# Optimization experiments

Hardware: AMD Instinct MI355X
Metric: run time of the kernel (lower is better)

Reference implementation:

```python
import jax, jax.numpy as jnp
import numpy as np

B, D = 200000, 128
K = 1024


def setup_inputs() -> dict:
    key = jax.random.key(0)
    k1, k2 = jax.random.split(key)
    x_BD = jax.random.normal(k1, (B, D), dtype=jnp.float32)
    codebook = jax.random.uniform(k2, (K, D), dtype=jnp.float32)
    return {"x_BD": x_BD, "codebook": codebook}


def reference(x_BD, codebook):
    x_sq_B1 = jnp.sum(x_BD * x_BD, axis=-1, keepdims=True)
    c_sq_K = jnp.sum(codebook * codebook, axis=-1)
    dists_BK = x_sq_B1 - 2.0 * jnp.einsum("bd,kd->bk", x_BD, codebook) + c_sq_K
    codes_B = jnp.argmin(dists_BK, axis=-1)  # [B] int
    quant_x_BD = codebook[codes_B]           # gather, [B, D]
    return quant_x_BD, codes_B
```

## Files before the change

kernel.cpp:

```cpp
#include <hip/hip_runtime.h>


typedef float v2f __attribute__((ext_vector_type(2)));

#define DDIM 128
#define KCODES 1024
#define BM 64
#define BN 128
#define DCH 32
#define NTILES (KCODES / BN)
#define NCHUNK (DDIM / DCH)

__global__ void csq_kernel(const float* __restrict__ cb, float* __restrict__ csq) {
    int k = blockIdx.x * blockDim.x + threadIdx.x;
    if (k >= KCODES) return;
    const float* __restrict__ c = cb + (long)k * DDIM;
    float s0 = 0.f, s1 = 0.f, s2 = 0.f, s3 = 0.f;
#pragma unroll
    for (int d = 0; d < DDIM; d += 4) {
        s0 = fmaf(c[d + 0], c[d + 0], s0);
        s1 = fmaf(c[d + 1], c[d + 1], s1);
        s2 = fmaf(c[d + 2], c[d + 2], s2);
        s3 = fmaf(c[d + 3], c[d + 3], s3);
    }
    csq[k] = (s0 + s1) + (s2 + s3);
}

__launch_bounds__(256, 3)
__global__ void vq_gemm_kernel(const float* __restrict__ x, const float* __restrict__ cb,
                               const float* __restrict__ csq, float* __restrict__ quant,
                               float* __restrict__ codes) {
    __shared__ float xs[DDIM * BM];
    __shared__ float cs[DCH * BN];
    __shared__ int win[BM];

    const int tid = threadIdx.x;
    const long r0 = (long)blockIdx.x * BM;

    {
        const int r = tid >> 2;
        const int qb = (tid & 3) * 8;
        const float* __restrict__ xrow = x + (r0 + r) * DDIM;
#pragma unroll
        for (int j = 0; j < 8; ++j) {
            const int q = qb + j;
            const float4 v = *(const float4*)(xrow + q * 4);
            xs[(q * 4 + 0) * BM + r] = v.x;
            xs[(q * 4 + 1) * BM + r] = v.y;
            xs[(q * 4 + 2) * BM + r] = v.z;
            xs[(q * 4 + 3) * BM + r] = v.w;
        }
    }
    __syncthreads();

    const int tr = tid >> 4;
    const int tc = tid & 15;

    float s[4][4];
#pragma unroll
    for (int a = 0; a < 4; ++a)
#pragma unroll
        for (int b = 0; b < 4; ++b) s[a][b] = 0.f;
#pragma unroll
    for (int d = 0; d < DDIM; d += 4) {
#pragma unroll
        for (int dd = 0; dd < 4; ++dd) {
            const float4 v = *(const float4*)&xs[(d + dd) * BM + tr * 4];
            s[dd][0] = fmaf(v.x, v.x, s[dd][0]);
            s[dd][1] = fmaf(v.y, v.y, s[dd][1]);
            s[dd][2] = fmaf(v.z, v.z, s[dd][2]);
            s[dd][3] = fmaf(v.w, v.w, s[dd][3]);
        }
    }
    float xsq[4];
#pragma unroll
    for (int i = 0; i < 4; ++i) xsq[i] = (s[0][i] + s[1][i]) + (s[2][i] + s[3][i]);

    float best[4];
    int bidx[4];
#pragma unroll
    for (int i = 0; i < 4; ++i) { best[i] = 3.4e38f; bidx[i] = 0; }

    for (int ct = 0; ct < NTILES; ++ct) {
        v2f acc[4][4];
#pragma unroll
        for (int i = 0; i < 4; ++i)
#pragma unroll
            for (int jj = 0; jj < 4; ++jj) acc[i][jj] = (v2f){0.f, 0.f};

        for (int dc = 0; dc < NCHUNK; ++dc) {
            __syncthreads();
            {
                const int k = tid >> 1;
                const int qb = (tid & 1) * 4;
                const float* __restrict__ crow =
                    cb + (long)(ct * BN + k) * DDIM + dc * DCH;
#pragma unroll
                for (int j = 0; j < 4; ++j) {
                    const int q = qb + j;
                    const float4 v = *(const float4*)(crow + q * 4);
                    cs[(q * 4 + 0) * BN + k] = v.x;
                    cs[(q * 4 + 1) * BN + k] = v.y;
                    cs[(q * 4 + 2) * BN + k] = v.z;
                    cs[(q * 4 + 3) * BN + k] = v.w;
                }
            }
            __syncthreads();
#pragma unroll
            for (int d = 0; d < DCH; ++d) {
                const float4 xa  = *(const float4*)&xs[(dc * DCH + d) * BM + tr * 4];
                const float4 ca  = *(const float4*)&cs[d * BN + tc * 4];
                const float4 cb2 = *(const float4*)&cs[d * BN + 64 + tc * 4];
                const float xv[4] = {xa.x, xa.y, xa.z, xa.w};
                v2f cv[4];
                cv[0] = (v2f){ca.x, ca.y};
                cv[1] = (v2f){ca.z, ca.w};
                cv[2] = (v2f){cb2.x, cb2.y};
                cv[3] = (v2f){cb2.z, cb2.w};
#pragma unroll
                for (int i = 0; i < 4; ++i) {
                    const v2f xb = (v2f){xv[i], xv[i]};
#pragma unroll
                    for (int jj = 0; jj < 4; ++jj)
                        acc[i][jj] = __builtin_elementwise_fma(xb, cv[jj], acc[i][jj]);
                }
            }
        }

        float csq_r[8];
#pragma unroll
        for (int j = 0; j < 4; ++j) {
            csq_r[j]     = csq[ct * BN + tc * 4 + j];
            csq_r[4 + j] = csq[ct * BN + 64 + tc * 4 + j];
        }
#pragma unroll
        for (int i = 0; i < 4; ++i) {
#pragma unroll
            for (int jj = 0; jj < 4; ++jj) {
#pragma unroll
                for (int h = 0; h < 2; ++h) {
                    const int jl = jj * 2 + h;
                    const int cj = ct * BN + ((jl < 4) ? (tc * 4 + jl) : (64 + tc * 4 + jl - 4));
                    const float dist = fmaf(-2.0f, acc[i][jj][h], xsq[i]) + csq_r[jl];
                    if (dist < best[i]) { best[i] = dist; bidx[i] = cj; }
                }
            }
        }
    }

    __syncthreads();
    float* redb = cs;
    int* redi = (int*)cs + BM * 16;
#pragma unroll
    for (int i = 0; i < 4; ++i) {
        const int r = tr * 4 + i;
        redb[r * 16 + tc] = best[i];
        redi[r * 16 + tc] = bidx[i];
    }
    __syncthreads();
    if (tid < BM) {
        float b = redb[tid * 16];
        int bi = redi[tid * 16];
#pragma unroll
        for (int e = 1; e < 16; ++e) {
            const float v = redb[tid * 16 + e];
            const int vi = redi[tid * 16 + e];
            if (v < b || (v == b && vi < bi)) { b = v; bi = vi; }
        }
        codes[r0 + tid] = (float)bi;
        win[tid] = bi;
    }
    __syncthreads();

    {
        const int r = tid >> 2;
        const int qb = (tid & 3) * 8;
        const float* __restrict__ crow = cb + (long)win[r] * DDIM;
        float* __restrict__ qrow = quant + (r0 + r) * DDIM;
#pragma unroll
        for (int j = 0; j < 8; ++j) {
            const int q = qb + j;
            *(float4*)(qrow + q * 4) = *(const float4*)(crow + q * 4);
        }
    }
}

extern "C" void kernel_launch(void* const* d_in, const int* in_sizes, int n_in,
                              void* d_out, int out_size, void* d_ws, size_t ws_size,
                              hipStream_t stream) {
    const float* x  = (const float*)d_in[0];
    const float* cb = (const float*)d_in[1];
    const int B = in_sizes[0] / DDIM;

    float* quant = (float*)d_out;
    float* codes = (float*)d_out + (size_t)B * DDIM;
    float* csq   = (float*)d_ws;

    csq_kernel<<<(KCODES + 255) / 256, 256, 0, stream>>>(cb, csq);

    const int blocks = B / BM;
    vq_gemm_kernel<<<blocks, 256, 0, stream>>>(x, cb, csq, quant, codes);
}
```

Before: 815.5 us.

## Rewrite VQ kernel with scalar-loaded x rows and transposed codebook streaming

```diff
diff --git a/kernel.cpp b/kernel.cpp
--- a/kernel.cpp
+++ b/kernel.cpp
@@ -2,14 +2,11 @@
 
 
 typedef float v2f __attribute__((ext_vector_type(2)));
+typedef int   v2i __attribute__((ext_vector_type(2)));
 
 #define DDIM 128
 #define KCODES 1024
-#define BM 64
-#define BN 128
-#define DCH 32
-#define NTILES (KCODES / BN)
-#define NCHUNK (DDIM / DCH)
+#define BMR 16
 
 __global__ void csq_kernel(const float* __restrict__ cb, float* __restrict__ csq) {
     int k = blockIdx.x * blockDim.x + threadIdx.x;
@@ -26,162 +23,167 @@
     csq[k] = (s0 + s1) + (s2 + s3);
 }
 
-__launch_bounds__(256, 3)
-__global__ void vq_gemm_kernel(const float* __restrict__ x, const float* __restrict__ cb,
-                               const float* __restrict__ csq, float* __restrict__ quant,
-                               float* __restrict__ codes) {
-    __shared__ float xs[DDIM * BM];
-    __shared__ float cs[DCH * BN];
-    __shared__ int win[BM];
+__global__ void ct_kernel(const float* __restrict__ cb, float* __restrict__ cT) {
+    const int idx = blockIdx.x * 256 + threadIdx.x;
+    const int d = idx >> 10, k = idx & 1023;
+    cT[idx] = cb[k * DDIM + d];
+}
+
+#define PKL(a, xx, cc) \
+    asm("v_pk_fma_f32 %0, %1, %2, %0 op_sel:[0,0,0] op_sel_hi:[0,1,1]" \
+        : "+v"(a) : "s"(xx), "v"(cc))
+#define PKH(a, xx, cc) \
+    asm("v_pk_fma_f32 %0, %1, %2, %0 op_sel:[1,0,0] op_sel_hi:[1,1,1]" \
+        : "+v"(a) : "s"(xx), "v"(cc))
+
+#define DECLX(S) v2i xq##S##0, xq##S##1, xq##S##2, xq##S##3, \
+                     xq##S##4, xq##S##5, xq##S##6, xq##S##7;
+
+#define ISSUE_X(S, xbp) do { const float* _xb = (xbp); \
+    asm volatile( \
+        "s_load_dwordx2 %[a0], %[xb], 0x0\n\t" \
+        "s_load_dwordx2 %[a1], %[xb], 0x200\n\t" \
+        "s_load_dwordx2 %[a2], %[xb], 0x400\n\t" \
+        "s_load_dwordx2 %[a3], %[xb], 0x600\n\t" \
+        "s_load_dwordx2 %[a4], %[xb], 0x800\n\t" \
+        "s_load_dwordx2 %[a5], %[xb], 0xa00\n\t" \
+        "s_load_dwordx2 %[a6], %[xb], 0xc00\n\t" \
+        "s_load_dwordx2 %[a7], %[xb], 0xe00" \
+        : [a0] "=s"(xq##S##0), [a1] "=s"(xq##S##1), \
+          [a2] "=s"(xq##S##2), [a3] "=s"(xq##S##3), \
+          [a4] "=s"(xq##S##4), [a5] "=s"(xq##S##5), \
+          [a6] "=s"(xq##S##6), [a7] "=s"(xq##S##7) \
+        : [xb] "s"(_xb)); } while (0)
+
+#define CROW_L(S, R) \
+    PKL(acc[R][0], xq##S##R, c##S##0); PKL(acc[R][1], xq##S##R, c##S##1); \
+    PKL(acc[R][2], xq##S##R, c##S##2); PKL(acc[R][3], xq##S##R, c##S##3);
+#define CROW_H(S, R) \
+    PKH(acc[R][0], xq##S##R, c##S##4); PKH(acc[R][1], xq##S##R, c##S##5); \
+    PKH(acc[R][2], xq##S##R, c##S##6); PKH(acc[R][3], xq##S##R, c##S##7);
+
+#define COMPUTE(S) do { \
+    CROW_L(S, 0) CROW_L(S, 1) CROW_L(S, 2) CROW_L(S, 3) \
+    CROW_L(S, 4) CROW_L(S, 5) CROW_L(S, 6) CROW_L(S, 7) \
+    CROW_H(S, 0) CROW_H(S, 1) CROW_H(S, 2) CROW_H(S, 3) \
+    CROW_H(S, 4) CROW_H(S, 5) CROW_H(S, 6) CROW_H(S, 7) } while (0)
+
+__launch_bounds__(256, 4)
+__global__ void vq_kernel(const float* __restrict__ x, const float* __restrict__ cb,
+                          const float* __restrict__ cT, const float* __restrict__ csq,
+                          float* __restrict__ quant, float* __restrict__ codes) {
+    __shared__ float xsqs[BMR];
+    __shared__ float redv[4][8];
+    __shared__ int   redi[4][8];
+    __shared__ int   win[BMR];
 
     const int tid = threadIdx.x;
-    const long r0 = (long)blockIdx.x * BM;
-
-    {
-        const int r = tid >> 2;
-        const int qb = (tid & 3) * 8;
-        const float* __restrict__ xrow = x + (r0 + r) * DDIM;
-#pragma unroll
-        for (int j = 0; j < 8; ++j) {
-            const int q = qb + j;
-            const float4 v = *(const float4*)(xrow + q * 4);
-            xs[(q * 4 + 0) * BM + r] = v.x;
-            xs[(q * 4 + 1) * BM + r] = v.y;
-            xs[(q * 4 + 2) * BM + r] = v.z;
-            xs[(q * 4 + 3) * BM + r] = v.w;
+    const int lane = tid & 63;
+    const int wv = __builtin_amdgcn_readfirstlane(tid >> 6);
+    const int rg = wv >> 1;
+    const int ch = wv & 1;
+    const long r0 = (long)blockIdx.x * BMR;
+
+    if (tid < BMR) {
+        const float* __restrict__ xr = x + (r0 + tid) * DDIM;
+        float s0 = 0.f, s1 = 0.f, s2 = 0.f, s3 = 0.f;
+#pragma unroll
+        for (int q = 0; q < 32; ++q) {
+            const float4 v = *(const float4*)(xr + q * 4);
+            s0 = fmaf(v.x, v.x, s0);
+            s1 = fmaf(v.y, v.y, s1);
+            s2 = fmaf(v.z, v.z, s2);
+            s3 = fmaf(v.w, v.w, s3);
         }
+        xsqs[tid] = (s0 + s1) + (s2 + s3);
     }
     __syncthreads();
 
-    const int tr = tid >> 4;
-    const int tc = tid & 15;
-
-    float s[4][4];
-#pragma unroll
-    for (int a = 0; a < 4; ++a)
-#pragma unroll
-        for (int b = 0; b < 4; ++b) s[a][b] = 0.f;
-#pragma unroll
-    for (int d = 0; d < DDIM; d += 4) {
-#pragma unroll
-        for (int dd = 0; dd < 4; ++dd) {
-            const float4 v = *(const float4*)&xs[(d + dd) * BM + tr * 4];
-            s[dd][0] = fmaf(v.x, v.x, s[dd][0]);
-            s[dd][1] = fmaf(v.y, v.y, s[dd][1]);
-            s[dd][2] = fmaf(v.z, v.z, s[dd][2]);
-            s[dd][3] = fmaf(v.w, v.w, s[dd][3]);
-        }
-    }
-    float xsq[4];
-#pragma unroll
-    for (int i = 0; i < 4; ++i) xsq[i] = (s[0][i] + s[1][i]) + (s[2][i] + s[3][i]);
-
-    float best[4];
-    int bidx[4];
-#pragma unroll
-    for (int i = 0; i < 4; ++i) { best[i] = 3.4e38f; bidx[i] = 0; }
-
-    for (int ct = 0; ct < NTILES; ++ct) {
-        v2f acc[4][4];
-#pragma unroll
-        for (int i = 0; i < 4; ++i)
-#pragma unroll
-            for (int jj = 0; jj < 4; ++jj) acc[i][jj] = (v2f){0.f, 0.f};
-
-        for (int dc = 0; dc < NCHUNK; ++dc) {
-            __syncthreads();
-            {
-                const int k = tid >> 1;
-                const int qb = (tid & 1) * 4;
-                const float* __restrict__ crow =
-                    cb + (long)(ct * BN + k) * DDIM + dc * DCH;
-#pragma unroll
-                for (int j = 0; j < 4; ++j) {
-                    const int q = qb + j;
-                    const float4 v = *(const float4*)(crow + q * 4);
-                    cs[(q * 4 + 0) * BN + k] = v.x;
-                    cs[(q * 4 + 1) * BN + k] = v.y;
-                    cs[(q * 4 + 2) * BN + k] = v.z;
-                    cs[(q * 4 + 3) * BN + k] = v.w;
-                }
-            }
-            __syncthreads();
-#pragma unroll
-            for (int d = 0; d < DCH; ++d) {
-                const float4 xa  = *(const float4*)&xs[(dc * DCH + d) * BM + tr * 4];
-                const float4 ca  = *(const float4*)&cs[d * BN + tc * 4];
-                const float4 cb2 = *(const float4*)&cs[d * BN + 64 + tc * 4];
-                const float xv[4] = {xa.x, xa.y, xa.z, xa.w};
-                v2f cv[4];
-                cv[0] = (v2f){ca.x, ca.y};
-                cv[1] = (v2f){ca.z, ca.w};
-                cv[2] = (v2f){cb2.x, cb2.y};
-                cv[3] = (v2f){cb2.z, cb2.w};
-#pragma unroll
-                for (int i = 0; i < 4; ++i) {
-                    const v2f xb = (v2f){xv[i], xv[i]};
-#pragma unroll
-                    for (int jj = 0; jj < 4; ++jj)
-                        acc[i][jj] = __builtin_elementwise_fma(xb, cv[jj], acc[i][jj]);
-                }
+    const float* __restrict__ xg = x + (r0 + rg * 8) * DDIM;
+    const int cbase = ch * 512 + lane * 8;
+    const float* __restrict__ cT0 = cT + cbase;
+
+    v2f acc[8][4];
+#pragma unroll
+    for (int r = 0; r < 8; ++r)
+#pragma unroll
+        for (int j = 0; j < 4; ++j) acc[r][j] = (v2f){0.f, 0.f};
+
+    DECLX(A) DECLX(B)
+    v2f cA0, cA1, cA2, cA3, cA4, cA5, cA6, cA7;
+    v2f cB0, cB1, cB2, cB3, cB4, cB5, cB6, cB7;
+
+    ISSUE_X(A, xg);
+    cA0 = *(const v2f*)(cT0);        cA1 = *(const v2f*)(cT0 + 2);
+    cA2 = *(const v2f*)(cT0 + 4);    cA3 = *(const v2f*)(cT0 + 6);
+    cA4 = *(const v2f*)(cT0 + 1024); cA5 = *(const v2f*)(cT0 + 1026);
+    cA6 = *(const v2f*)(cT0 + 1028); cA7 = *(const v2f*)(cT0 + 1030);
+    asm volatile("s_waitcnt lgkmcnt(0)" ::: "memory");
+    __builtin_amdgcn_sched_barrier(0);
+
+#define STEP(CUR, NXT, pp) do { \
+    const int np = ((pp) < 63) ? ((pp) + 1) : 63; \
+    ISSUE_X(NXT, xg + np * 2); \
+    const float* _ct = cT0 + (long)np * 2048; \
+    c##NXT##0 = *(const v2f*)(_ct);        c##NXT##1 = *(const v2f*)(_ct + 2); \
+    c##NXT##2 = *(const v2f*)(_ct + 4);    c##NXT##3 = *(const v2f*)(_ct + 6); \
+    c##NXT##4 = *(const v2f*)(_ct + 1024); c##NXT##5 = *(const v2f*)(_ct + 1026); \
+    c##NXT##6 = *(const v2f*)(_ct + 1028); c##NXT##7 = *(const v2f*)(_ct + 1030); \
+    COMPUTE(CUR); \
+    asm volatile("s_waitcnt lgkmcnt(0)" ::: "memory"); \
+    __builtin_amdgcn_sched_barrier(0); \
+} while (0)
+
+#pragma unroll 1
+    for (int p = 0; p < 64; p += 2) {
+        STEP(A, B, p);
+        STEP(B, A, p + 1);
+    }
+#undef STEP
+
+    const float4 cqa = *(const float4*)(csq + cbase);
+    const float4 cqb = *(const float4*)(csq + cbase + 4);
+    const float cqv[8] = {cqa.x, cqa.y, cqa.z, cqa.w, cqb.x, cqb.y, cqb.z, cqb.w};
+#pragma unroll
+    for (int r = 0; r < 8; ++r) {
+        const float xr = xsqs[rg * 8 + r];
+        float b = 3.4e38f; int bi = 0;
+#pragma unroll
+        for (int j = 0; j < 4; ++j) {
+#pragma unroll
+            for (int h = 0; h < 2; ++h) {
+                const float dist = fmaf(-2.0f, acc[r][j][h], xr) + cqv[j * 2 + h];
+                const int idx = cbase + j * 2 + h;
+                if (dist < b) { b = dist; bi = idx; }
             }
         }
-
-        float csq_r[8];
-#pragma unroll
-        for (int j = 0; j < 4; ++j) {
-            csq_r[j]     = csq[ct * BN + tc * 4 + j];
-            csq_r[4 + j] = csq[ct * BN + 64 + tc * 4 + j];
+#pragma unroll
+        for (int off = 32; off >= 1; off >>= 1) {
+            const float ov = __shfl_xor(b, off);
+            const int oi = __shfl_xor(bi, off);
+            if (ov < b || (ov == b && oi < bi)) { b = ov; bi = oi; }
         }
-#pragma unroll
-        for (int i = 0; i < 4; ++i) {
-#pragma unroll
-            for (int jj = 0; jj < 4; ++jj) {
-#pragma unroll
-                for (int h = 0; h < 2; ++h) {
-                    const int jl = jj * 2 + h;
-                    const int cj = ct * BN + ((jl < 4) ? (tc * 4 + jl) : (64 + tc * 4 + jl - 4));
-                    const float dist = fmaf(-2.0f, acc[i][jj][h], xsq[i]) + csq_r[jl];
-                    if (dist < best[i]) { best[i] = dist; bidx[i] = cj; }
-                }
-            }
-        }
-    }
-
+        if (lane == 0) { redv[wv][r] = b; redi[wv][r] = bi; }
+    }
     __syncthreads();
-    float* redb = cs;
-    int* redi = (int*)cs + BM * 16;
-#pragma unroll
-    for (int i = 0; i < 4; ++i) {
-        const int r = tr * 4 + i;
-        redb[r * 16 + tc] = best[i];
-        redi[r * 16 + tc] = bidx[i];
-    }
-    __syncthreads();
-    if (tid < BM) {
-        float b = redb[tid * 16];
-        int bi = redi[tid * 16];
-#pragma unroll
-        for (int e = 1; e < 16; ++e) {
-            const float v = redb[tid * 16 + e];
-            const int vi = redi[tid * 16 + e];
-            if (v < b || (v == b && vi < bi)) { b = v; bi = vi; }
-        }
+
+    if (tid < BMR) {
+        const int g = tid >> 3, rl = tid & 7;
+        float b = redv[g * 2][rl]; int bi = redi[g * 2][rl];
+        const float v = redv[g * 2 + 1][rl]; const int vi = redi[g * 2 + 1][rl];
+        if (v < b || (v == b && vi < bi)) { b = v; bi = vi; }
         codes[r0 + tid] = (float)bi;
         win[tid] = bi;
     }
     __syncthreads();
 
     {
-        const int r = tid >> 2;
-        const int qb = (tid & 3) * 8;
-        const float* __restrict__ crow = cb + (long)win[r] * DDIM;
-        float* __restrict__ qrow = quant + (r0 + r) * DDIM;
-#pragma unroll
-        for (int j = 0; j < 8; ++j) {
-            const int q = qb + j;
-            *(float4*)(qrow + q * 4) = *(const float4*)(crow + q * 4);
-        }
+        const int r = tid >> 4;
+        const int s = (tid & 15) * 8;
+        const float* __restrict__ crow = cb + (long)win[r] * DDIM + s;
+        float* __restrict__ qrow = quant + (r0 + r) * DDIM + s;
+        *(float4*)(qrow) = *(const float4*)(crow);
+        *(float4*)(qrow + 4) = *(const float4*)(crow + 4);
     }
 }
 
@@ -195,9 +197,11 @@
     float* quant = (float*)d_out;
     float* codes = (float*)d_out + (size_t)B * DDIM;
     float* csq   = (float*)d_ws;
+    float* cT    = (float*)d_ws + KCODES;
 
     csq_kernel<<<(KCODES + 255) / 256, 256, 0, stream>>>(cb, csq);
-
-    const int blocks = B / BM;
-    vq_gemm_kernel<<<blocks, 256, 0, stream>>>(x, cb, csq, quant, codes);
-}
+    ct_kernel<<<(DDIM * KCODES) / 256, 256, 0, stream>>>(cb, cT);
+
+    const int blocks = B / BMR;
+    vq_kernel<<<blocks, 256, 0, stream>>>(x, cb, cT, csq, quant, codes);
+}
```

Measured after the change: 709.7 us. -13.0%, faster.
